# Performance work log

Measured on AMD Instinct MI355X. Metric: run time of the kernel, lower is better.

The kernel has to match this reference:

```python
import jax, jax.numpy as jnp
import numpy as np

B, T, N, F_IN = 4, 16, 1000, 8
E = 8000
HID = 64
HEADS = 4
L = 5


def setup_inputs() -> dict:
    key = jax.random.key(0)
    ks = jax.random.split(key, 16)
    s = 0.1
    return {
        "x_seq": jax.random.normal(ks[0], (B, T, N, F_IN), dtype=jnp.float32),
        "edge_index": jax.random.randint(ks[1], (2, E), 0, N, dtype=jnp.int32),
        "edge_weight": jax.random.uniform(ks[2], (E,), dtype=jnp.float32),
        # input projection
        "W_in": jax.random.normal(ks[3], (F_IN, HID)) * s,
        "b_in": jnp.zeros((HID,), jnp.float32),
        # 5 stacked GATConv layers (heads=4, concat=False -> per-head dim = HID, mean over heads)
        "Wg": jax.random.normal(ks[4], (L, HID, HEADS * HID)) * s,
        "a_src": jax.random.normal(ks[5], (L, HEADS, HID)) * s,
        "a_dst": jax.random.normal(ks[6], (L, HEADS, HID)) * s,
        "bg": jnp.zeros((L, HID), jnp.float32),
        # GRU (input = N*HID flattened node features, torch gate order r,z,n)
        "W_ih": jax.random.normal(ks[7], (3 * HID, N * HID)) * 0.02,
        "W_hh": jax.random.normal(ks[8], (3 * HID, HID)) * s,
        "b_ih": jnp.zeros((3 * HID,), jnp.float32),
        "b_hh": jnp.zeros((3 * HID,), jnp.float32),
        # head: Linear(hidden_dim, num_nodes*pred_window) so out.view(B, N) works
        "W_fc": jax.random.normal(ks[9], (HID, N)) * s,
        "b_fc": jnp.zeros((N,), jnp.float32),
    }


def reference(x_seq, edge_index, edge_weight, W_in, b_in, Wg, a_src, a_dst, bg,
              W_ih, W_hh, b_ih, b_hh, W_fc, b_fc):
    Bb, Tt, Nn, Fin = x_seq.shape
    hid = W_in.shape[1]
    heads = a_src.shape[1]
    # PyG GATConv adds self-loops by default
    self_loops = jnp.arange(Nn, dtype=edge_index.dtype)
    src = jnp.concatenate([edge_index[0], self_loops])
    dst = jnp.concatenate([edge_index[1], self_loops])

    # input_fc over all (batch*seq*node) rows
    x = (x_seq.reshape(-1, Fin) @ W_in + b_in).reshape(Bb * Tt, Nn, hid)

    def gat_one(x_g, W, asrc, adst, b):
        h = (x_g @ W).reshape(Nn, heads, hid)            # [N,H,C]
        ls = (h * asrc).sum(-1)                          # [N,H] src attention terms
        ld = (h * adst).sum(-1)                          # [N,H] dst attention terms
        e = jax.nn.leaky_relu(ls[src] + ld[dst], 0.2)    # [E',H]
        m = jax.ops.segment_max(e, dst, num_segments=Nn)
        ex = jnp.exp(e - m[dst])
        den = jax.ops.segment_sum(ex, dst, num_segments=Nn)
        alpha = ex / (den[dst] + 1e-16)                  # softmax over incoming edges
        msg = alpha[:, :, None] * h[src]                 # [E',H,C]
        agg = jax.ops.segment_sum(msg, dst, num_segments=Nn)
        return agg.mean(axis=1) + b                      # concat=False -> mean heads

    for l in range(Wg.shape[0]):
        x = jax.nn.elu(jax.vmap(
            lambda xg, W=Wg[l], a1=a_src[l], a2=a_dst[l], b=bg[l]: gat_one(xg, W, a1, a2, b)
        )(x))

    # GRU over time, input = flattened node features per timestep
    seq = x.reshape(Bb, Tt, Nn * hid).transpose(1, 0, 2)  # [T,B,N*HID]

    def step(h, x_t):
        gi = x_t @ W_ih.T + b_ih
        gh = h @ W_hh.T + b_hh
        ir, iz, inn = jnp.split(gi, 3, axis=-1)
        hr, hz, hn = jnp.split(gh, 3, axis=-1)
        r = jax.nn.sigmoid(ir + hr)
        z = jax.nn.sigmoid(iz + hz)
        n = jnp.tanh(inn + r * hn)
        return (1.0 - z) * n + z * h, None

    h0 = jnp.zeros((Bb, hid), x_seq.dtype)
    hT, _ = jax.lax.scan(step, h0, seq)                  # last GRU output == final h
    return hT @ W_fc + b_fc                              # [B, N]
```

## Files before the change

kernel.cpp:

```cpp
#include <hip/hip_runtime.h>
#include <math.h>

#define NB 4
#define TT 16
#define NNODE 1000
#define FIN 8
#define EE 8000
#define EP 9000
#define EPAD 16384
#define HID 64
#define HEADS 4
#define NL 5
#define GG (NB*TT)
#define ROWS (GG*NNODE)
#define HCOL (HEADS*HID)
#define KGI (NNODE*HID)
#define GOUT 192
#define GIK 128
#define KSPLIT (KGI/GIK)
#define GOSZ (GG*GOUT)
#define WPSZ (8*4*64*8)

typedef unsigned short u16;
typedef __attribute__((ext_vector_type(8))) short short8;
typedef __attribute__((ext_vector_type(4))) float f32x4;

__device__ inline u16 f2bf(float f) {
    unsigned int u = __float_as_uint(f);
    unsigned int r = u + 0x7FFFu + ((u >> 16) & 1u);
    return (u16)(r >> 16);
}
__device__ inline float bf2f(u16 h) {
    return __uint_as_float(((unsigned int)h) << 16);
}
__device__ inline ushort4 bfhi4(float4 a) {
    ushort4 r; r.x = f2bf(a.x); r.y = f2bf(a.y); r.z = f2bf(a.z); r.w = f2bf(a.w); return r;
}
__device__ inline ushort4 bflo4(float4 a, ushort4 h) {
    ushort4 r;
    r.x = f2bf(a.x - bf2f(h.x)); r.y = f2bf(a.y - bf2f(h.y));
    r.z = f2bf(a.z - bf2f(h.z)); r.w = f2bf(a.w - bf2f(h.w));
    return r;
}

__global__ void k_build_edges(const int* __restrict__ eidx, int* __restrict__ src_e,
                              int* __restrict__ dst_e, int* __restrict__ deg, int* __restrict__ fill) {
    int i = blockIdx.x * blockDim.x + threadIdx.x;
    if (i < EP) {
        int s, d;
        if (i < EE) { s = eidx[i]; d = eidx[EE + i]; }
        else { s = i - EE; d = i - EE; }
        src_e[i] = s; dst_e[i] = d;
    }
    if (i < NNODE) { deg[i] = 0; fill[i] = 0; }
}

__global__ void k_csr_count(const int* __restrict__ dst_e, int* __restrict__ deg) {
    int i = blockIdx.x * blockDim.x + threadIdx.x;
    if (i < EP) atomicAdd(&deg[dst_e[i]], 1);
}

__global__ __launch_bounds__(256) void k_csr_scan(const int* __restrict__ deg, int* __restrict__ rowptr_p) {
    __shared__ int s[1024];
    int tid = threadIdx.x;
    for (int i = tid; i < 1024; i += 256) s[i] = (i < NNODE) ? ((deg[i] + 7) & ~7) : 0;
    __syncthreads();
    for (int off = 1; off < 1024; off <<= 1) {
        int t[4];
        #pragma unroll
        for (int q = 0; q < 4; q++) { int i = tid + 256 * q; t[q] = (i >= off) ? s[i - off] : 0; }
        __syncthreads();
        #pragma unroll
        for (int q = 0; q < 4; q++) { int i = tid + 256 * q; s[i] += t[q]; }
        __syncthreads();
    }
    for (int i = tid; i < NNODE; i += 256) rowptr_p[i + 1] = s[i];
    if (tid == 0) rowptr_p[0] = 0;
}

__global__ void k_csr_fill(const int* __restrict__ src_e, const int* __restrict__ dst_e,
                           const int* __restrict__ rowptr_p, const int* __restrict__ deg,
                           int* __restrict__ fill, int* __restrict__ csr_src) {
    int i = blockIdx.x * blockDim.x + threadIdx.x;
    if (i < EP) {
        int d = dst_e[i];
        int pos = atomicAdd(&fill[d], 1);
        csr_src[rowptr_p[d] + pos] = src_e[i];
    }
    if (i < NNODE) {
        int rs = rowptr_p[i], re = rowptr_p[i + 1];
        for (int j = rs + deg[i]; j < re; j++) csr_src[j] = i;
    }
}

__global__ void k_wa(const float* __restrict__ Wg, const float* __restrict__ a_src,
                     const float* __restrict__ a_dst, float* __restrict__ wa, float* __restrict__ wd) {
    int t = blockIdx.x * 256 + threadIdx.x;
    if (t >= 2 * NL * HID * HEADS) return;
    int kind = t >= NL * HID * HEADS;
    int u = t - kind * NL * HID * HEADS;
    int l = u >> 8;
    int rem = u & 255;
    int j = rem >> 2, hd = rem & 3;
    const float* a = (kind ? a_dst : a_src) + (size_t)l * HCOL + hd * HID;
    const float* Wl = Wg + (size_t)l * HID * HCOL + (size_t)j * HCOL + hd * HID;
    float acc = 0.f;
    #pragma unroll 8
    for (int c = 0; c < HID; c++) acc += Wl[c] * a[c];
    float* out = kind ? wd : wa;
    out[(size_t)l * HCOL + j * 4 + hd] = acc;
}

__global__ void k_wpack(const float* __restrict__ Wg, u16* __restrict__ wph, u16* __restrict__ wpl) {
    int t = blockIdx.x * 256 + threadIdx.x;
    if (t >= NL * WPSZ) return;
    int j    = t & 7;
    int lane = (t >> 3) & 63;
    int ct   = (t >> 9) & 3;
    int ks   = (t >> 11) & 7;
    int l    = t >> 14;
    int k = ks * 32 + (lane >> 4) * 8 + j;
    int c = ct * 16 + (lane & 15);
    float v = Wg[(size_t)l * HID * HCOL + (size_t)(k & 63) * HCOL + (k >> 6) * 64 + c];
    u16 h = f2bf(v);
    wph[t] = h;
    wpl[t] = f2bf(v - bf2f(h));
}

__global__ void k_input_fc(const float* __restrict__ xseq, const float4* __restrict__ Win4,
                           const float4* __restrict__ b_in4, const float4* __restrict__ wa04,
                           const float4* __restrict__ wd04, float4* __restrict__ x0,
                           float4* __restrict__ ls4, float4* __restrict__ ld4) {
    int idx = blockIdx.x * 256 + threadIdx.x;
    int r = idx >> 4, c4 = idx & 15;
    float4 acc = b_in4[c4];
    #pragma unroll
    for (int k = 0; k < FIN; k++) {
        float xv = xseq[r * FIN + k];
        float4 w = Win4[k * 16 + c4];
        acc.x += xv * w.x; acc.y += xv * w.y; acc.z += xv * w.z; acc.w += xv * w.w;
    }
    x0[idx] = acc;
    float xr[4] = {acc.x, acc.y, acc.z, acc.w};
    float4 pls = make_float4(0.f, 0.f, 0.f, 0.f);
    float4 pld = make_float4(0.f, 0.f, 0.f, 0.f);
    #pragma unroll
    for (int jj = 0; jj < 4; jj++) {
        float4 wa_j = wa04[c4 * 4 + jj];
        float4 wd_j = wd04[c4 * 4 + jj];
        pls.x += xr[jj] * wa_j.x; pls.y += xr[jj] * wa_j.y;
        pls.z += xr[jj] * wa_j.z; pls.w += xr[jj] * wa_j.w;
        pld.x += xr[jj] * wd_j.x; pld.y += xr[jj] * wd_j.y;
        pld.z += xr[jj] * wd_j.z; pld.w += xr[jj] * wd_j.w;
    }
    #pragma unroll
    for (int o = 1; o < 16; o <<= 1) {
        pls.x += __shfl_xor(pls.x, o, 64); pls.y += __shfl_xor(pls.y, o, 64);
        pls.z += __shfl_xor(pls.z, o, 64); pls.w += __shfl_xor(pls.w, o, 64);
        pld.x += __shfl_xor(pld.x, o, 64); pld.y += __shfl_xor(pld.y, o, 64);
        pld.z += __shfl_xor(pld.z, o, 64); pld.w += __shfl_xor(pld.w, o, 64);
    }
    if (c4 == 0) {
        ls4[r] = pls;
        ld4[r] = pld;
    }
}

__global__ __launch_bounds__(256) void k_gat_fused(
        const float4* __restrict__ x4, const float4* __restrict__ ls4, const float4* __restrict__ ld4,
        const int* __restrict__ rowptr_p, const int* __restrict__ csr_src, const int* __restrict__ deg,
        const u16* __restrict__ wph, const u16* __restrict__ wpl, const float* __restrict__ bg,
        float* __restrict__ xout, const float4* __restrict__ wa4, const float4* __restrict__ wd4,
        float4* __restrict__ lso4, float4* __restrict__ ldo4) {
    __shared__ u16 yhs[32][264];
    __shared__ u16 yls[32][264];
    __shared__ float s_e[4][4][264];
    __shared__ unsigned short s_src[4][4][64];
    __shared__ float s_den[4][4][4];
    int b = blockIdx.x;
    int xcd = b & 7, sb = b >> 3;
    int g = xcd + 8 * (sb >> 5);
    int nb = (sb & 31) * 32;
    int tid = threadIdx.x;
    int wid = tid >> 6, lane = tid & 63;
    int nsub = lane >> 4;
    int j0 = lane & 15;
    int c4 = lane & 15;
    const float4* lsg = ls4 + (size_t)g * NNODE;
    const float4* xg = x4 + (size_t)g * NNODE * 16 + c4;

    for (int it2 = 0; it2 < 2; it2++) {
        __syncthreads();
        int n_l = wid * 8 + it2 * 4 + nsub;
        int n_s = nb + n_l;
        int valid = n_s < NNODE;
        int n_c = valid ? n_s : (NNODE - 1);
        int rs = rowptr_p[n_c];
        int dgp = valid ? (rowptr_p[n_c + 1] - rs) : 0;
        int dg = valid ? deg[n_c] : 0;
        int dg16 = (dgp + 15) & ~15;
        if (dg16 > 64) dg16 = 64;
        if (dgp > 64) dgp = 64;
        if (dg > 64) dg = 64;
        float4 ldv = ld4[(size_t)g * NNODE + n_c];

        float4 mx = make_float4(-1e30f, -1e30f, -1e30f, -1e30f);
        for (int base = 0; base < dg16; base += 16) {
            int j = base + j0;
            int sv = n_c;
            if (j < dgp) sv = csr_src[rs + j];
            s_src[wid][nsub][j] = (unsigned short)sv;
            float4 lo = make_float4(-1e30f, -1e30f, -1e30f, -1e30f);
            if (j < dg) {
                float4 t = lsg[sv];
                t.x += ldv.x; t.y += ldv.y; t.z += ldv.z; t.w += ldv.w;
                t.x = fmaxf(t.x, 0.2f * t.x); t.y = fmaxf(t.y, 0.2f * t.y);
                t.z = fmaxf(t.z, 0.2f * t.z); t.w = fmaxf(t.w, 0.2f * t.w);
                lo = t;
                mx.x = fmaxf(mx.x, lo.x); mx.y = fmaxf(mx.y, lo.y);
                mx.z = fmaxf(mx.z, lo.z); mx.w = fmaxf(mx.w, lo.w);
            }
            *reinterpret_cast<float4*>(&s_e[wid][nsub][j * 4]) = lo;
        }
        #pragma unroll
        for (int o = 1; o < 16; o <<= 1) {
            mx.x = fmaxf(mx.x, __shfl_xor(mx.x, o, 64));
            mx.y = fmaxf(mx.y, __shfl_xor(mx.y, o, 64));
            mx.z = fmaxf(mx.z, __shfl_xor(mx.z, o, 64));
            mx.w = fmaxf(mx.w, __shfl_xor(mx.w, o, 64));
        }
        float4 den = make_float4(0.f, 0.f, 0.f, 0.f);
        for (int base = 0; base < dg16; base += 16) {
            int j = base + j0;
            float4 e = make_float4(0.f, 0.f, 0.f, 0.f);
            if (j < dg) {
                float4 lo = *reinterpret_cast<const float4*>(&s_e[wid][nsub][j * 4]);
                e.x = __expf(lo.x - mx.x);
                e.y = __expf(lo.y - mx.y);
                e.z = __expf(lo.z - mx.z);
                e.w = __expf(lo.w - mx.w);
            }
            den.x += e.x; den.y += e.y; den.z += e.z; den.w += e.w;
            *reinterpret_cast<float4*>(&s_e[wid][nsub][j * 4]) = e;
        }
        #pragma unroll
        for (int o = 1; o < 16; o <<= 1) {
            den.x += __shfl_xor(den.x, o, 64);
            den.y += __shfl_xor(den.y, o, 64);
            den.z += __shfl_xor(den.z, o, 64);
            den.w += __shfl_xor(den.w, o, 64);
        }
        if (j0 == 0) *reinterpret_cast<float4*>(&s_den[wid][nsub][0]) = den;
        __syncthreads();

        float4 a0 = make_float4(0.f, 0.f, 0.f, 0.f);
        float4 a1 = a0, a2 = a0, a3 = a0;
        const float* ep = &s_e[wid][nsub][0];
        const unsigned short* sp = &s_src[wid][nsub][0];
        int dg4 = (dg + 3) & ~3;
        int q = 0;
        for (; q + 8 <= dg4; q += 8) {
            int sj[8]; float4 ev[8], xv[8];
            #pragma unroll
            for (int u = 0; u < 8; u++) sj[u] = sp[q + u];
            #pragma unroll
            for (int u = 0; u < 8; u++) xv[u] = xg[(size_t)sj[u] * 16];
            #pragma unroll
            for (int u = 0; u < 8; u++) ev[u] = *reinterpret_cast<const float4*>(&ep[(q + u) * 4]);
            #pragma unroll
            for (int u = 0; u < 8; u++) {
                a0.x += ev[u].x * xv[u].x; a0.y += ev[u].x * xv[u].y;
                a0.z += ev[u].x * xv[u].z; a0.w += ev[u].x * xv[u].w;
                a1.x += ev[u].y * xv[u].x; a1.y += ev[u].y * xv[u].y;
                a1.z += ev[u].y * xv[u].z; a1.w += ev[u].y * xv[u].w;
                a2.x += ev[u].z * xv[u].x; a2.y += ev[u].z * xv[u].y;
                a2.z += ev[u].z * xv[u].z; a2.w += ev[u].z * xv[u].w;
                a3.x += ev[u].w * xv[u].x; a3.y += ev[u].w * xv[u].y;
                a3.z += ev[u].w * xv[u].z; a3.w += ev[u].w * xv[u].w;
            }
        }
        if (q < dg4) {
            int sj[4]; float4 ev[4], xv[4];
            #pragma unroll
            for (int u = 0; u < 4; u++) sj[u] = sp[q + u];
            #pragma unroll
            for (int u = 0; u < 4; u++) xv[u] = xg[(size_t)sj[u] * 16];
            #pragma unroll
            for (int u = 0; u < 4; u++) ev[u] = *reinterpret_cast<const float4*>(&ep[(q + u) * 4]);
            #pragma unroll
            for (int u = 0; u < 4; u++) {
                a0.x += ev[u].x * xv[u].x; a0.y += ev[u].x * xv[u].y;
                a0.z += ev[u].x * xv[u].z; a0.w += ev[u].x * xv[u].w;
                a1.x += ev[u].y * xv[u].x; a1.y += ev[u].y * xv[u].y;
                a1.z += ev[u].y * xv[u].z; a1.w += ev[u].y * xv[u].w;
                a2.x += ev[u].z * xv[u].x; a2.y += ev[u].z * xv[u].y;
                a2.z += ev[u].z * xv[u].z; a2.w += ev[u].z * xv[u].w;
                a3.x += ev[u].w * xv[u].x; a3.y += ev[u].w * xv[u].y;
                a3.z += ev[u].w * xv[u].z; a3.w += ev[u].w * xv[u].w;
            }
        }
        float4 dv = *reinterpret_cast<const float4*>(&s_den[wid][nsub][0]);
        float i0 = 1.f / (dv.x + 1e-16f), i1 = 1.f / (dv.y + 1e-16f);
        float i2 = 1.f / (dv.z + 1e-16f), i3 = 1.f / (dv.w + 1e-16f);
        a0.x *= i0; a0.y *= i0; a0.z *= i0; a0.w *= i0;
        a1.x *= i1; a1.y *= i1; a1.z *= i1; a1.w *= i1;
        a2.x *= i2; a2.y *= i2; a2.z *= i2; a2.w *= i2;
        a3.x *= i3; a3.y *= i3; a3.z *= i3; a3.w *= i3;
        ushort4 h0 = bfhi4(a0), h1 = bfhi4(a1), h2 = bfhi4(a2), h3 = bfhi4(a3);
        *reinterpret_cast<ushort4*>(&yhs[n_l][0 * 64 + c4 * 4]) = h0;
        *reinterpret_cast<ushort4*>(&yhs[n_l][1 * 64 + c4 * 4]) = h1;
        *reinterpret_cast<ushort4*>(&yhs[n_l][2 * 64 + c4 * 4]) = h2;
        *reinterpret_cast<ushort4*>(&yhs[n_l][3 * 64 + c4 * 4]) = h3;
        *reinterpret_cast<ushort4*>(&yls[n_l][0 * 64 + c4 * 4]) = bflo4(a0, h0);
        *reinterpret_cast<ushort4*>(&yls[n_l][1 * 64 + c4 * 4]) = bflo4(a1, h1);
        *reinterpret_cast<ushort4*>(&yls[n_l][2 * 64 + c4 * 4]) = bflo4(a2, h2);
        *reinterpret_cast<ushort4*>(&yls[n_l][3 * 64 + c4 * 4]) = bflo4(a3, h3);
    }
    __syncthreads();

    int r0l = (wid & 1) * 16;
    int ch = wid >> 1;
    int arow = lane & 15, kg = lane >> 4;
    f32x4 acc0 = {0.f, 0.f, 0.f, 0.f};
    f32x4 acc1 = {0.f, 0.f, 0.f, 0.f};
    const short8* bh8 = reinterpret_cast<const short8*>(wph) + lane;
    const short8* bl8 = reinterpret_cast<const short8*>(wpl) + lane;
    #pragma unroll
    for (int ks = 0; ks < 8; ks++) {
        short8 ah = *reinterpret_cast<const short8*>(&yhs[r0l + arow][ks * 32 + kg * 8]);
        short8 al = *reinterpret_cast<const short8*>(&yls[r0l + arow][ks * 32 + kg * 8]);
        #pragma unroll
        for (int ctl = 0; ctl < 2; ctl++) {
            int ctg = ch * 2 + ctl;
            short8 bh = bh8[(size_t)(ks * 4 + ctg) * 64];
            short8 bl = bl8[(size_t)(ks * 4 + ctg) * 64];
            f32x4* ac = ctl ? &acc1 : &acc0;
            *ac = __builtin_amdgcn_mfma_f32_16x16x32_bf16(ah, bh, *ac, 0, 0, 0);
            *ac = __builtin_amdgcn_mfma_f32_16x16x32_bf16(ah, bl, *ac, 0, 0, 0);
            *ac = __builtin_amdgcn_mfma_f32_16x16x32_bf16(al, bh, *ac, 0, 0, 0);
        }
    }

    float ev2[2][4];
    #pragma unroll
    for (int ctl = 0; ctl < 2; ctl++) {
        int c = (ch * 2 + ctl) * 16 + arow;
        float bc = bg[c];
        f32x4 a = ctl ? acc1 : acc0;
        #pragma unroll
        for (int r = 0; r < 4; r++) {
            int node = nb + r0l + kg * 4 + r;
            float v = a[r] * 0.25f + bc;
            float e = v > 0.f ? v : expm1f(v);
            ev2[ctl][r] = e;
            if (node < NNODE)
                xout[((size_t)g * NNODE + node) * HID + c] = e;
        }
    }
    if (wa4) {
        float* s_part = &s_e[0][0][0];
        __syncthreads();
        #pragma unroll
        for (int r = 0; r < 4; r++) {
            float4 pls = make_float4(0.f, 0.f, 0.f, 0.f);
            float4 pld = make_float4(0.f, 0.f, 0.f, 0.f);
            #pragma unroll
            for (int ctl = 0; ctl < 2; ctl++) {
                int c = (ch * 2 + ctl) * 16 + arow;
                float e = ev2[ctl][r];
                float4 wa_c = wa4[c];
                float4 wd_c = wd4[c];
                pls.x += e * wa_c.x; pls.y += e * wa_c.y;
                pls.z += e * wa_c.z; pls.w += e * wa_c.w;
                pld.x += e * wd_c.x; pld.y += e * wd_c.y;
                pld.z += e * wd_c.z; pld.w += e * wd_c.w;
            }
            #pragma unroll
            for (int o = 1; o < 16; o <<= 1) {
                pls.x += __shfl_xor(pls.x, o, 64); pls.y += __shfl_xor(pls.y, o, 64);
                pls.z += __shfl_xor(pls.z, o, 64); pls.w += __shfl_xor(pls.w, o, 64);
                pld.x += __shfl_xor(pld.x, o, 64); pld.y += __shfl_xor(pld.y, o, 64);
                pld.z += __shfl_xor(pld.z, o, 64); pld.w += __shfl_xor(pld.w, o, 64);
            }
            if (arow == 0) {
                int rl = r0l + kg * 4 + r;
                float4* p = reinterpret_cast<float4*>(&s_part[(ch * 32 + rl) * 8]);
                p[0] = pls; p[1] = pld;
            }
        }
        __syncthreads();
        int rl = tid >> 3, cc = tid & 7;
        int node = nb + rl;
        if (node < NNODE) {
            float v = s_part[rl * 8 + cc] + s_part[(32 + rl) * 8 + cc];
            float* dst = (cc < 4) ? reinterpret_cast<float*>(lso4) : reinterpret_cast<float*>(ldo4);
            dst[((size_t)g * NNODE + node) * 4 + (cc & 3)] = v;
        }
    }
}

__global__ __launch_bounds__(256) void k_gi_gemm(const float* __restrict__ x, const float* __restrict__ W_ih,
                                                 float* __restrict__ gip) {
    __shared__ float xs[32 * 68];
    __shared__ float ws[32 * 196];
    int k0 = blockIdx.x * GIK;
    int tid = threadIdx.x;
    int lane = tid & 63;
    int wv = tid >> 6;
    int tx = tid & 15, ty = tid >> 4;
    float4 accs[4][3];
    #pragma unroll
    for (int i = 0; i < 4; i++)
        #pragma unroll
        for (int j = 0; j < 3; j++) accs[i][j] = make_float4(0.f, 0.f, 0.f, 0.f);

    for (int kt = 0; kt < GIK / 32; kt++) {
        int kb = k0 + kt * 32;
        #pragma unroll
        for (int it = 0; it < 2; it++) {
            int kq = wv + 4 * it;
            float4 v = *reinterpret_cast<const float4*>(&x[(size_t)lane * KGI + kb + kq * 4]);
            int k = kq * 4;
            xs[(k + 0) * 68 + lane] = v.x;
            xs[(k + 1) * 68 + lane] = v.y;
            xs[(k + 2) * 68 + lane] = v.z;
            xs[(k + 3) * 68 + lane] = v.w;
        }
        #pragma unroll
        for (int cg = 0; cg < 3; cg++) {
            #pragma unroll
            for (int it = 0; it < 2; it++) {
                int kq = wv + 4 * it;
                int c = cg * 64 + lane;
                float4 v = *reinterpret_cast<const float4*>(&W_ih[(size_t)c * KGI + kb + kq * 4]);
                int k = kq * 4;
                ws[(k + 0) * 196 + c] = v.x;
                ws[(k + 1) * 196 + c] = v.y;
                ws[(k + 2) * 196 + c] = v.z;
                ws[(k + 3) * 196 + c] = v.w;
            }
        }
        __syncthreads();
        for (int kk = 0; kk < 32; kk++) {
            float4 xv = *reinterpret_cast<const float4*>(&xs[kk * 68 + ty * 4]);
            float4 w0 = *reinterpret_cast<const float4*>(&ws[kk * 196 + tx * 4]);
            float4 w1 = *reinterpret_cast<const float4*>(&ws[kk * 196 + 64 + tx * 4]);
            float4 w2 = *reinterpret_cast<const float4*>(&ws[kk * 196 + 128 + tx * 4]);
            #pragma unroll
            for (int i = 0; i < 4; i++) {
                float xi = (i == 0) ? xv.x : (i == 1) ? xv.y : (i == 2) ? xv.z : xv.w;
                accs[i][0].x += xi * w0.x; accs[i][0].y += xi * w0.y; accs[i][0].z += xi * w0.z; accs[i][0].w += xi * w0.w;
                accs[i][1].x += xi * w1.x; accs[i][1].y += xi * w1.y; accs[i][1].z += xi * w1.z; accs[i][1].w += xi * w1.w;
                accs[i][2].x += xi * w2.x; accs[i][2].y += xi * w2.y; accs[i][2].z += xi * w2.z; accs[i][2].w += xi * w2.w;
            }
        }
        __syncthreads();
    }
    float* out = gip + (size_t)blockIdx.x * GOSZ;
    #pragma unroll
    for (int i = 0; i < 4; i++)
        #pragma unroll
        for (int j = 0; j < 3; j++)
            *reinterpret_cast<float4*>(&out[(ty * 4 + i) * GOUT + j * 64 + tx * 4]) = accs[i][j];
}

__global__ void k_gi_reduce1(const float* __restrict__ gip, float* __restrict__ gip2) {
    int idx = blockIdx.x * 256 + threadIdx.x;
    const float* p = gip + (size_t)blockIdx.y * 50 * GOSZ + idx;
    float a = 0.f;
    #pragma unroll 5
    for (int s = 0; s < 50; s++) a += p[(size_t)s * GOSZ];
    gip2[blockIdx.y * GOSZ + idx] = a;
}

__global__ void k_gi_reduce2(const float* __restrict__ gip2, const float* __restrict__ b_ih,
                             float* __restrict__ gi) {
    int idx = blockIdx.x * 256 + threadIdx.x;
    float a = b_ih[idx % GOUT];
    #pragma unroll
    for (int y = 0; y < 10; y++) a += gip2[(size_t)y * GOSZ + idx];
    gi[idx] = a;
}

__global__ __launch_bounds__(192) void k_gru(const float* __restrict__ gi, const float* __restrict__ W_hh,
                                             const float* __restrict__ b_hh, float* __restrict__ hT) {
    __shared__ float hs[64];
    __shared__ float gh[192];
    int j = threadIdx.x;
    int b = blockIdx.x;
    float wrow[64];
    #pragma unroll
    for (int q = 0; q < 16; q++) {
        float4 v = *reinterpret_cast<const float4*>(&W_hh[(size_t)j * 64 + q * 4]);
        wrow[q * 4 + 0] = v.x; wrow[q * 4 + 1] = v.y;
        wrow[q * 4 + 2] = v.z; wrow[q * 4 + 3] = v.w;
    }
    float bj = b_hh[j];
    if (j < 64) hs[j] = 0.f;
    __syncthreads();
    for (int t = 0; t < TT; t++) {
        float a0 = 0.f, a1 = 0.f, a2 = 0.f, a3 = 0.f;
        #pragma unroll
        for (int q = 0; q < 16; q++) {
            float4 h4 = *reinterpret_cast<const float4*>(&hs[q * 4]);
            a0 += h4.x * wrow[q * 4 + 0];
            a1 += h4.y * wrow[q * 4 + 1];
            a2 += h4.z * wrow[q * 4 + 2];
            a3 += h4.w * wrow[q * 4 + 3];
        }
        gh[j] = bj + ((a0 + a1) + (a2 + a3));
        __syncthreads();
        if (j < 64) {
            int row = (b * TT + t) * GOUT;
            float ir = gi[row + j], iz = gi[row + 64 + j], in_ = gi[row + 128 + j];
            float r = 1.f / (1.f + expf(-(ir + gh[j])));
            float z = 1.f / (1.f + expf(-(iz + gh[64 + j])));
            float nv = tanhf(in_ + r * gh[128 + j]);
            hs[j] = (1.f - z) * nv + z * hs[j];
        }
        __syncthreads();
    }
    if (j < 64) hT[b * 64 + j] = hs[j];
}

__global__ void k_final(const float* __restrict__ hT, const float* __restrict__ W_fc,
                        const float* __restrict__ b_fc, float* __restrict__ out) {
    int idx = blockIdx.x * 256 + threadIdx.x;
    if (idx >= NB * NNODE) return;
    int b = idx / NNODE, n = idx % NNODE;
    float acc = b_fc[n];
    #pragma unroll
    for (int c = 0; c < HID; c++) acc += hT[b * HID + c] * W_fc[c * NNODE + n];
    out[idx] = acc;
}

extern "C" void kernel_launch(void* const* d_in, const int* in_sizes, int n_in,
                              void* d_out, int out_size, void* d_ws, size_t ws_size,
                              hipStream_t stream) {
    const float* x_seq  = (const float*)d_in[0];
    const int*   eidx   = (const int*)  d_in[1];
    const float* W_in   = (const float*)d_in[3];
    const float* b_in   = (const float*)d_in[4];
    const float* Wg     = (const float*)d_in[5];
    const float* a_src  = (const float*)d_in[6];
    const float* a_dst  = (const float*)d_in[7];
    const float* bg     = (const float*)d_in[8];
    const float* W_ih   = (const float*)d_in[9];
    const float* W_hh   = (const float*)d_in[10];
    const float* b_ih   = (const float*)d_in[11];
    const float* b_hh   = (const float*)d_in[12];
    const float* W_fc   = (const float*)d_in[13];
    const float* b_fc   = (const float*)d_in[14];
    float* out = (float*)d_out;

    float* wsf = (float*)d_ws;
    size_t off = 0;
    float* x0a    = wsf + off; off += (size_t)ROWS * HID;
    float* x0b    = wsf + off; off += (size_t)ROWS * HID;
    float* lsa    = wsf + off; off += (size_t)ROWS * HEADS;
    float* ldaf   = wsf + off; off += (size_t)ROWS * HEADS;
    float* lsbf   = wsf + off; off += (size_t)ROWS * HEADS;
    float* ldbf   = wsf + off; off += (size_t)ROWS * HEADS;
    float* wab    = wsf + off; off += NL * HCOL;
    float* wdb    = wsf + off; off += NL * HCOL;
    float* gib    = wsf + off; off += GOSZ;
    float* hTb    = wsf + off; off += 256;
    u16* wphb     = (u16*)(wsf + off); off += NL * WPSZ / 2;
    u16* wplb     = (u16*)(wsf + off); off += NL * WPSZ / 2;
    float* gip    = wsf + off; off += (size_t)KSPLIT * GOSZ;
    float* gip2   = wsf + off; off += 10 * GOSZ;
    int* ib = (int*)(wsf + off);
    int* src_e    = ib;          ib += EP;
    int* dst_e    = ib;          ib += EP;
    int* rowptr_p = ib;          ib += NNODE + 1;
    int* csr_src  = ib;          ib += EPAD;
    int* deg      = ib;          ib += NNODE;
    int* fill     = ib;          ib += NNODE;

    k_build_edges<<<(EP + 255) / 256, 256, 0, stream>>>(eidx, src_e, dst_e, deg, fill);
    k_csr_count<<<(EP + 255) / 256, 256, 0, stream>>>(dst_e, deg);
    k_csr_scan<<<1, 256, 0, stream>>>(deg, rowptr_p);
    k_csr_fill<<<(EP + 255) / 256, 256, 0, stream>>>(src_e, dst_e, rowptr_p, deg, fill, csr_src);

    k_wa<<<10, 256, 0, stream>>>(Wg, a_src, a_dst, wab, wdb);
    k_wpack<<<(NL * WPSZ + 255) / 256, 256, 0, stream>>>(Wg, wphb, wplb);

    k_input_fc<<<ROWS * 16 / 256, 256, 0, stream>>>(
        x_seq, (const float4*)W_in, (const float4*)b_in,
        (const float4*)wab, (const float4*)wdb, (float4*)x0a, (float4*)lsa, (float4*)ldaf);

    float* xc = x0a;  float* xn = x0b;
    float* lsc = lsa; float* ldc = ldaf;
    float* lsn = lsbf; float* ldn = ldbf;
    for (int l = 0; l < NL; l++) {
        const float4* wa_next = (l + 1 < NL) ? (const float4*)(wab + (size_t)(l + 1) * HCOL) : nullptr;
        const float4* wd_next = (l + 1 < NL) ? (const float4*)(wdb + (size_t)(l + 1) * HCOL) : nullptr;
        k_gat_fused<<<2048, 256, 0, stream>>>(
            (const float4*)xc, (const float4*)lsc, (const float4*)ldc,
            rowptr_p, csr_src, deg,
            wphb + (size_t)l * WPSZ, wplb + (size_t)l * WPSZ, bg + (size_t)l * HID,
            xn, wa_next, wd_next, (float4*)lsn, (float4*)ldn);
        float* t;
        t = xc; xc = xn; xn = t;
        t = lsc; lsc = lsn; lsn = t;
        t = ldc; ldc = ldn; ldn = t;
    }

    k_gi_gemm<<<KSPLIT, 256, 0, stream>>>(xc, W_ih, gip);
    k_gi_reduce1<<<dim3(GOSZ / 256, 10), 256, 0, stream>>>(gip, gip2);
    k_gi_reduce2<<<GOSZ / 256, 256, 0, stream>>>(gip2, b_ih, gib);
    k_gru<<<4, 192, 0, stream>>>(gib, W_hh, b_hh, hTb);
    k_final<<<(NB * NNODE + 255) / 256, 256, 0, stream>>>(hTb, W_fc, b_fc, out);
}
```

Baseline: 414.4 us.

## Halve GAT block node tile to 16 nodes and launch 63 blocks per graph

Each fused GAT block now handles 16 nodes instead of 32, so the two-iteration aggregation loop collapses to one pass. The grid grows from 2048 to 64*63 blocks and the old 1000/32 tail waste shrinks. In the MFMA projection each wave now computes one 16-column tile over all 16 rows, and the attention-term partials are reduced across four waves instead of two. This gives more parallelism, less shared memory and fewer barriers per block, at the cost of more blocks and reloading the packed weights in twice as many blocks.

After: 418.0 us. About the same (+0.9%).

```diff
diff --git a/kernel.cpp b/kernel.cpp
--- a/kernel.cpp
+++ b/kernel.cpp
@@ -20,6 +20,7 @@
 #define KSPLIT (KGI/GIK)
 #define GOSZ (GG*GOUT)
 #define WPSZ (8*4*64*8)
+#define NBLK 63
 
 typedef unsigned short u16;
 typedef __attribute__((ext_vector_type(8))) short short8;
@@ -172,15 +173,15 @@
         const u16* __restrict__ wph, const u16* __restrict__ wpl, const float* __restrict__ bg,
         float* __restrict__ xout, const float4* __restrict__ wa4, const float4* __restrict__ wd4,
         float4* __restrict__ lso4, float4* __restrict__ ldo4) {
-    __shared__ u16 yhs[32][264];
-    __shared__ u16 yls[32][264];
+    __shared__ u16 yhs[16][264];
+    __shared__ u16 yls[16][264];
     __shared__ float s_e[4][4][264];
-    __shared__ unsigned short s_src[4][4][64];
+    __shared__ u16 s_src[4][4][64];
     __shared__ float s_den[4][4][4];
     int b = blockIdx.x;
     int xcd = b & 7, sb = b >> 3;
-    int g = xcd + 8 * (sb >> 5);
-    int nb = (sb & 31) * 32;
+    int g = xcd + 8 * (sb / NBLK);
+    int nb = (sb % NBLK) * 16;
     int tid = threadIdx.x;
     int wid = tid >> 6, lane = tid & 63;
     int nsub = lane >> 4;
@@ -189,74 +190,72 @@
     const float4* lsg = ls4 + (size_t)g * NNODE;
     const float4* xg = x4 + (size_t)g * NNODE * 16 + c4;
 
-    for (int it2 = 0; it2 < 2; it2++) {
-        __syncthreads();
-        int n_l = wid * 8 + it2 * 4 + nsub;
-        int n_s = nb + n_l;
-        int valid = n_s < NNODE;
-        int n_c = valid ? n_s : (NNODE - 1);
-        int rs = rowptr_p[n_c];
-        int dgp = valid ? (rowptr_p[n_c + 1] - rs) : 0;
-        int dg = valid ? deg[n_c] : 0;
-        int dg16 = (dgp + 15) & ~15;
-        if (dg16 > 64) dg16 = 64;
-        if (dgp > 64) dgp = 64;
-        if (dg > 64) dg = 64;
-        float4 ldv = ld4[(size_t)g * NNODE + n_c];
-
-        float4 mx = make_float4(-1e30f, -1e30f, -1e30f, -1e30f);
-        for (int base = 0; base < dg16; base += 16) {
-            int j = base + j0;
-            int sv = n_c;
-            if (j < dgp) sv = csr_src[rs + j];
-            s_src[wid][nsub][j] = (unsigned short)sv;
-            float4 lo = make_float4(-1e30f, -1e30f, -1e30f, -1e30f);
-            if (j < dg) {
-                float4 t = lsg[sv];
-                t.x += ldv.x; t.y += ldv.y; t.z += ldv.z; t.w += ldv.w;
-                t.x = fmaxf(t.x, 0.2f * t.x); t.y = fmaxf(t.y, 0.2f * t.y);
-                t.z = fmaxf(t.z, 0.2f * t.z); t.w = fmaxf(t.w, 0.2f * t.w);
-                lo = t;
-                mx.x = fmaxf(mx.x, lo.x); mx.y = fmaxf(mx.y, lo.y);
-                mx.z = fmaxf(mx.z, lo.z); mx.w = fmaxf(mx.w, lo.w);
-            }
-            *reinterpret_cast<float4*>(&s_e[wid][nsub][j * 4]) = lo;
-        }
-        #pragma unroll
-        for (int o = 1; o < 16; o <<= 1) {
-            mx.x = fmaxf(mx.x, __shfl_xor(mx.x, o, 64));
-            mx.y = fmaxf(mx.y, __shfl_xor(mx.y, o, 64));
-            mx.z = fmaxf(mx.z, __shfl_xor(mx.z, o, 64));
-            mx.w = fmaxf(mx.w, __shfl_xor(mx.w, o, 64));
-        }
-        float4 den = make_float4(0.f, 0.f, 0.f, 0.f);
-        for (int base = 0; base < dg16; base += 16) {
-            int j = base + j0;
-            float4 e = make_float4(0.f, 0.f, 0.f, 0.f);
-            if (j < dg) {
-                float4 lo = *reinterpret_cast<const float4*>(&s_e[wid][nsub][j * 4]);
-                e.x = __expf(lo.x - mx.x);
-                e.y = __expf(lo.y - mx.y);
-                e.z = __expf(lo.z - mx.z);
-                e.w = __expf(lo.w - mx.w);
-            }
-            den.x += e.x; den.y += e.y; den.z += e.z; den.w += e.w;
-            *reinterpret_cast<float4*>(&s_e[wid][nsub][j * 4]) = e;
-        }
-        #pragma unroll
-        for (int o = 1; o < 16; o <<= 1) {
-            den.x += __shfl_xor(den.x, o, 64);
-            den.y += __shfl_xor(den.y, o, 64);
-            den.z += __shfl_xor(den.z, o, 64);
-            den.w += __shfl_xor(den.w, o, 64);
-        }
-        if (j0 == 0) *reinterpret_cast<float4*>(&s_den[wid][nsub][0]) = den;
-        __syncthreads();
-
+    int n_l = wid * 4 + nsub;
+    int n_s = nb + n_l;
+    int valid = n_s < NNODE;
+    int n_c = valid ? n_s : (NNODE - 1);
+    int rs = rowptr_p[n_c];
+    int dgp = valid ? (rowptr_p[n_c + 1] - rs) : 0;
+    int dg = valid ? deg[n_c] : 0;
+    int dg16 = (dgp + 15) & ~15;
+    if (dg16 > 64) dg16 = 64;
+    if (dgp > 64) dgp = 64;
+    if (dg > 64) dg = 64;
+    float4 ldv = ld4[(size_t)g * NNODE + n_c];
+
+    float4 mx = make_float4(-1e30f, -1e30f, -1e30f, -1e30f);
+    for (int base = 0; base < dg16; base += 16) {
+        int j = base + j0;
+        int sv = n_c;
+        if (j < dgp) sv = csr_src[rs + j];
+        s_src[wid][nsub][j] = (u16)sv;
+        float4 lo = make_float4(-1e30f, -1e30f, -1e30f, -1e30f);
+        if (j < dg) {
+            float4 t = lsg[sv];
+            t.x += ldv.x; t.y += ldv.y; t.z += ldv.z; t.w += ldv.w;
+            t.x = fmaxf(t.x, 0.2f * t.x); t.y = fmaxf(t.y, 0.2f * t.y);
+            t.z = fmaxf(t.z, 0.2f * t.z); t.w = fmaxf(t.w, 0.2f * t.w);
+            lo = t;
+            mx.x = fmaxf(mx.x, lo.x); mx.y = fmaxf(mx.y, lo.y);
+            mx.z = fmaxf(mx.z, lo.z); mx.w = fmaxf(mx.w, lo.w);
+        }
+        *reinterpret_cast<float4*>(&s_e[wid][nsub][j * 4]) = lo;
+    }
+    #pragma unroll
+    for (int o = 1; o < 16; o <<= 1) {
+        mx.x = fmaxf(mx.x, __shfl_xor(mx.x, o, 64));
+        mx.y = fmaxf(mx.y, __shfl_xor(mx.y, o, 64));
+        mx.z = fmaxf(mx.z, __shfl_xor(mx.z, o, 64));
+        mx.w = fmaxf(mx.w, __shfl_xor(mx.w, o, 64));
+    }
+    float4 den = make_float4(0.f, 0.f, 0.f, 0.f);
+    for (int base = 0; base < dg16; base += 16) {
+        int j = base + j0;
+        float4 e = make_float4(0.f, 0.f, 0.f, 0.f);
+        if (j < dg) {
+            float4 lo = *reinterpret_cast<const float4*>(&s_e[wid][nsub][j * 4]);
+            e.x = __expf(lo.x - mx.x);
+            e.y = __expf(lo.y - mx.y);
+            e.z = __expf(lo.z - mx.z);
+            e.w = __expf(lo.w - mx.w);
+        }
+        den.x += e.x; den.y += e.y; den.z += e.z; den.w += e.w;
+        *reinterpret_cast<float4*>(&s_e[wid][nsub][j * 4]) = e;
+    }
+    #pragma unroll
+    for (int o = 1; o < 16; o <<= 1) {
+        den.x += __shfl_xor(den.x, o, 64);
+        den.y += __shfl_xor(den.y, o, 64);
+        den.z += __shfl_xor(den.z, o, 64);
+        den.w += __shfl_xor(den.w, o, 64);
+    }
+    if (j0 == 0) *reinterpret_cast<float4*>(&s_den[wid][nsub][0]) = den;
+
+    {
         float4 a0 = make_float4(0.f, 0.f, 0.f, 0.f);
         float4 a1 = a0, a2 = a0, a3 = a0;
         const float* ep = &s_e[wid][nsub][0];
-        const unsigned short* sp = &s_src[wid][nsub][0];
+        const u16* sp = &s_src[wid][nsub][0];
         int dg4 = (dg + 3) & ~3;
         int q = 0;
         for (; q + 8 <= dg4; q += 8) {
@@ -318,56 +317,44 @@
     }
     __syncthreads();
 
-    int r0l = (wid & 1) * 16;
-    int ch = wid >> 1;
     int arow = lane & 15, kg = lane >> 4;
     f32x4 acc0 = {0.f, 0.f, 0.f, 0.f};
-    f32x4 acc1 = {0.f, 0.f, 0.f, 0.f};
     const short8* bh8 = reinterpret_cast<const short8*>(wph) + lane;
     const short8* bl8 = reinterpret_cast<const short8*>(wpl) + lane;
     #pragma unroll
     for (int ks = 0; ks < 8; ks++) {
-        short8 ah = *reinterpret_cast<const short8*>(&yhs[r0l + arow][ks * 32 + kg * 8]);
-        short8 al = *reinterpret_cast<const short8*>(&yls[r0l + arow][ks * 32 + kg * 8]);
-        #pragma unroll
-        for (int ctl = 0; ctl < 2; ctl++) {
-            int ctg = ch * 2 + ctl;
-            short8 bh = bh8[(size_t)(ks * 4 + ctg) * 64];
-            short8 bl = bl8[(size_t)(ks * 4 + ctg) * 64];
-            f32x4* ac = ctl ? &acc1 : &acc0;
-            *ac = __builtin_amdgcn_mfma_f32_16x16x32_bf16(ah, bh, *ac, 0, 0, 0);
-            *ac = __builtin_amdgcn_mfma_f32_16x16x32_bf16(ah, bl, *ac, 0, 0, 0);
-            *ac = __builtin_amdgcn_mfma_f32_16x16x32_bf16(al, bh, *ac, 0, 0, 0);
-        }
-    }
-
-    float ev2[2][4];
-    #pragma unroll
-    for (int ctl = 0; ctl < 2; ctl++) {
-        int c = (ch * 2 + ctl) * 16 + arow;
+        short8 ah = *reinterpret_cast<const short8*>(&yhs[arow][ks * 32 + kg * 8]);
+        short8 al = *reinterpret_cast<const short8*>(&yls[arow][ks * 32 + kg * 8]);
+        short8 bh = bh8[(size_t)(ks * 4 + wid) * 64];
+        short8 bl = bl8[(size_t)(ks * 4 + wid) * 64];
+        acc0 = __builtin_amdgcn_mfma_f32_16x16x32_bf16(ah, bh, acc0, 0, 0, 0);
+        acc0 = __builtin_amdgcn_mfma_f32_16x16x32_bf16(ah, bl, acc0, 0, 0, 0);
+        acc0 = __builtin_amdgcn_mfma_f32_16x16x32_bf16(al, bh, acc0, 0, 0, 0);
+    }
+
+    float ev2[4];
+    {
+        int c = wid * 16 + arow;
         float bc = bg[c];
-        f32x4 a = ctl ? acc1 : acc0;
         #pragma unroll
         for (int r = 0; r < 4; r++) {
-            int node = nb + r0l + kg * 4 + r;
-            float v = a[r] * 0.25f + bc;
+            int node = nb + kg * 4 + r;
+            float v = acc0[r] * 0.25f + bc;
             float e = v > 0.f ? v : expm1f(v);
-            ev2[ctl][r] = e;
+            ev2[r] = e;
             if (node < NNODE)
                 xout[((size_t)g * NNODE + node) * HID + c] = e;
         }
     }
     if (wa4) {
         float* s_part = &s_e[0][0][0];
-        __syncthreads();
         #pragma unroll
         for (int r = 0; r < 4; r++) {
             float4 pls = make_float4(0.f, 0.f, 0.f, 0.f);
             float4 pld = make_float4(0.f, 0.f, 0.f, 0.f);
-            #pragma unroll
-            for (int ctl = 0; ctl < 2; ctl++) {
-                int c = (ch * 2 + ctl) * 16 + arow;
-                float e = ev2[ctl][r];
+            {
+                int c = wid * 16 + arow;
+                float e = ev2[r];
                 float4 wa_c = wa4[c];
                 float4 wd_c = wd4[c];
                 pls.x += e * wa_c.x; pls.y += e * wa_c.y;
@@ -383,18 +370,21 @@
                 pld.z += __shfl_xor(pld.z, o, 64); pld.w += __shfl_xor(pld.w, o, 64);
             }
             if (arow == 0) {
-                int rl = r0l + kg * 4 + r;
-                float4* p = reinterpret_cast<float4*>(&s_part[(ch * 32 + rl) * 8]);
+                int rl = kg * 4 + r;
+                float4* p = reinterpret_cast<float4*>(&s_part[(wid * 16 + rl) * 8]);
                 p[0] = pls; p[1] = pld;
             }
         }
         __syncthreads();
-        int rl = tid >> 3, cc = tid & 7;
-        int node = nb + rl;
-        if (node < NNODE) {
-            float v = s_part[rl * 8 + cc] + s_part[(32 + rl) * 8 + cc];
-            float* dst = (cc < 4) ? reinterpret_cast<float*>(lso4) : reinterpret_cast<float*>(ldo4);
-            dst[((size_t)g * NNODE + node) * 4 + (cc & 3)] = v;
+        if (tid < 128) {
+            int rl = tid >> 3, cc = tid & 7;
+            int node = nb + rl;
+            if (node < NNODE) {
+                float v = s_part[(0 * 16 + rl) * 8 + cc] + s_part[(1 * 16 + rl) * 8 + cc]
+                        + s_part[(2 * 16 + rl) * 8 + cc] + s_part[(3 * 16 + rl) * 8 + cc];
+                float* dst = (cc < 4) ? reinterpret_cast<float*>(lso4) : reinterpret_cast<float*>(ldo4);
+                dst[((size_t)g * NNODE + node) * 4 + (cc & 3)] = v;
+            }
         }
     }
 }
@@ -595,7 +585,7 @@
     for (int l = 0; l < NL; l++) {
         const float4* wa_next = (l + 1 < NL) ? (const float4*)(wab + (size_t)(l + 1) * HCOL) : nullptr;
         const float4* wd_next = (l + 1 < NL) ? (const float4*)(wdb + (size_t)(l + 1) * HCOL) : nullptr;
-        k_gat_fused<<<2048, 256, 0, stream>>>(
+        k_gat_fused<<<GG * NBLK, 256, 0, stream>>>(
             (const float4*)xc, (const float4*)lsc, (const float4*)ldc,
             rowptr_p, csr_src, deg,
             wphb + (size_t)l * WPSZ, wplb + (size_t)l * WPSZ, bg + (size_t)l * HID,
```
